# Kernel tuning notes

Measured on AMD Instinct MI355X. Metric: run time of the kernel, lower is better.

The kernel has to match this reference:

```python
import jax, jax.numpy as jnp
import numpy as np

N_COARSE = 12500
N_FINE = 50000
MIN_BASIS = 16  # (min(L_in, L_out) + 1) ** 2 with L_in = L_out = 3


def setup_inputs() -> dict:
    key = jax.random.key(0)
    ks = jax.random.split(key, 8)
    return {
        "last_inv": jax.random.normal(ks[0], (N_COARSE, 256), dtype=jnp.float32),
        "cur_inv": jax.random.normal(ks[1], (N_FINE, 256), dtype=jnp.float32),
        "last_equ": jax.random.normal(ks[2], (N_COARSE, 16, 256), dtype=jnp.float32),
        "cur_equ": jax.random.normal(ks[3], (N_FINE, 16, 256), dtype=jnp.float32),
        "upsampling": jax.random.randint(ks[4], (N_FINE,), 0, N_COARSE, dtype=jnp.int32),
        # Linear weights stored as [in, out] (torch weight is [out, in]; x @ W.T == x @ W_in_out)
        "W_last_equ": jax.random.normal(ks[5], (256, 256), dtype=jnp.float32) * 0.02,
        "W_cur_equ": jax.random.normal(ks[6], (256, 256), dtype=jnp.float32) * 0.02,
        "W_mlp": jax.random.normal(ks[7], (768, 512), dtype=jnp.float32) * 0.02,
    }


def reference(last_inv, cur_inv, last_equ, cur_equ, upsampling, W_last_equ, W_cur_equ, W_mlp):
    # nearest_upsample: gather coarse rows up to fine resolution
    li = jnp.take(last_inv, upsampling, axis=0)                 # [N_fine, 256]
    le = jnp.take(last_equ, upsampling, axis=0)[:, :MIN_BASIS]  # [N_fine, 16, 256]
    le = jnp.einsum('nbc,cd->nbd', le, W_last_equ)              # fc_last_equ (no bias)
    ce = jnp.einsum('nbc,cd->nbd', cur_equ[:, :MIN_BASIS], W_cur_equ)  # fc_cur_equ
    equ = (ce * le).mean(axis=1)                                # [N_fine, 256]
    com = jnp.concatenate([li, cur_inv, equ], axis=-1)          # [N_fine, 768]
    return com @ W_mlp                                          # LastUnaryBlock: Linear, no bias
```

## Files before the change

kernel.cpp:

```cpp
#include <hip/hip_runtime.h>
#include <hip/hip_bf16.h>

#define N_COARSE 12500
#define N_FINE   50000

typedef __bf16 bf16x8 __attribute__((ext_vector_type(8)));
typedef __bf16 bf16x4 __attribute__((ext_vector_type(4)));
typedef float  f32x4  __attribute__((ext_vector_type(4)));


__device__ __forceinline__ bf16x8 cvt8(f32x4 x, f32x4 y) {
    bf16x8 r;
    r[0] = (__bf16)x[0]; r[1] = (__bf16)x[1]; r[2] = (__bf16)x[2]; r[3] = (__bf16)x[3];
    r[4] = (__bf16)y[0]; r[5] = (__bf16)y[1]; r[6] = (__bf16)y[2]; r[7] = (__bf16)y[3];
    return r;
}

__device__ __forceinline__ int swz(int row, int byte) { return byte ^ ((row & 7) << 4); }

__device__ __forceinline__ void st_a(__bf16* lds, int row, int cs, bf16x8 v) {
    *(bf16x8*)((char*)lds + swz(row, row * 512 + cs * 16)) = v;
}
__device__ __forceinline__ bf16x8 ld_a(const __bf16* lds, int row, int ka) {
    return *(const bf16x8*)((const char*)lds + swz(row, row * 512 + ka * 2));
}

template<int NT>
__device__ __forceinline__ void stage_f32(const float* __restrict__ A, long row0,
                                          __bf16* lds, int tid, long maxrow) {
    const int r0 = tid >> 5, cs = tid & 31;
    constexpr int RPI = NT / 32;
    #pragma unroll
    for (int i = 0; i < 64 / RPI; ++i) {
        int row = r0 + i * RPI;
        long gr = row0 + row; if (gr > maxrow) gr = maxrow;
        const float* p = A + gr * 256 + cs * 8;
        f32x4 x = *(const f32x4*)p, y = *(const f32x4*)(p + 4);
        st_a(lds, row, cs, cvt8(x, y));
    }
}

__device__ __forceinline__ void mfma_tile(const __bf16* lds, const bf16x8* __restrict__ packB,
                                          int N, int c0, int ksb,
                                          f32x4 (&acc)[4][4], int lane) {
    const int g = lane >> 4, r15 = lane & 15;
    #pragma unroll
    for (int ks = 0; ks < 8; ++ks) {
        bf16x8 a[4];
        #pragma unroll
        for (int rt = 0; rt < 4; ++rt)
            a[rt] = ld_a(lds, rt * 16 + r15, ks * 32 + g * 8);
        const size_t kb = (size_t)((ksb + ks) * 4 + g) * N;
        #pragma unroll
        for (int ct = 0; ct < 4; ++ct) {
            bf16x8 b = packB[kb + c0 + ct * 16 + r15];
            #pragma unroll
            for (int rt = 0; rt < 4; ++rt)
                acc[rt][ct] = __builtin_amdgcn_mfma_f32_16x16x32_bf16(a[rt], b, acc[rt][ct], 0, 0, 0);
        }
    }
}

__global__ __launch_bounds__(256) void k_pack(const float* __restrict__ W,
                                              __bf16* __restrict__ dst, int K, int N) {
    int idx = blockIdx.x * 256 + threadIdx.x;
    if (idx >= K * N) return;
    int k = idx / N, n = idx % N;
    dst[((size_t)(k >> 3) * N + n) * 8 + (k & 7)] = (__bf16)W[(size_t)k * N + n];
}

__global__ __launch_bounds__(256) void k_cvt(const float* __restrict__ src,
                                             __bf16* __restrict__ dst, int n4) {
    int i = blockIdx.x * 256 + threadIdx.x;
    if (i >= n4) return;
    f32x4 v = ((const f32x4*)src)[i];
    bf16x4 o;
    o[0] = (__bf16)v[0]; o[1] = (__bf16)v[1]; o[2] = (__bf16)v[2]; o[3] = (__bf16)v[3];
    ((bf16x4*)dst)[i] = o;
}

__global__ __launch_bounds__(256) void k_coarse_equ(
    const float* __restrict__ last_equ, const bf16x8* __restrict__ packW,
    __bf16* __restrict__ LEp)
{
    __shared__ __attribute__((aligned(16))) __bf16 As[64 * 256];
    const int tid = threadIdx.x, lane = tid & 63, wid = tid >> 6;
    const long row0 = (long)blockIdx.x * 64;
    stage_f32<256>(last_equ, row0, As, tid, (long)N_COARSE * 16 - 1);
    __syncthreads();
    f32x4 acc[4][4] = {};
    mfma_tile(As, packW, 256, wid * 64, 0, acc, lane);
    #pragma unroll
    for (int rt = 0; rt < 4; ++rt) {
        int coarse = (int)(row0 >> 4) + rt;
        #pragma unroll
        for (int ct = 0; ct < 4; ++ct) {
            int cg = wid * 4 + ct;
            bf16x4 v;
            v[0] = (__bf16)acc[rt][ct][0]; v[1] = (__bf16)acc[rt][ct][1];
            v[2] = (__bf16)acc[rt][ct][2]; v[3] = (__bf16)acc[rt][ct][3];
            *(bf16x4*)(LEp + ((size_t)(coarse * 16 + cg) * 64 + lane) * 4) = v;
        }
    }
}

__global__ __launch_bounds__(256) void k_fine_equ(
    const float* __restrict__ cur_equ, const bf16x8* __restrict__ packW,
    const __bf16* __restrict__ LEp, const int* __restrict__ up,
    __bf16* __restrict__ equ)
{
    __shared__ __attribute__((aligned(16))) __bf16 As[64 * 256];
    const int tid = threadIdx.x, lane = tid & 63, wid = tid >> 6;
    const int n0 = blockIdx.x * 4;
    const long row0 = (long)blockIdx.x * 64;

    int cu[4];
    #pragma unroll
    for (int rt = 0; rt < 4; ++rt) cu[rt] = up[n0 + rt];

    stage_f32<256>(cur_equ, row0, As, tid, (long)N_FINE * 16 - 1);

    bf16x4 le[4][4];
    #pragma unroll
    for (int rt = 0; rt < 4; ++rt)
        #pragma unroll
        for (int ct = 0; ct < 4; ++ct)
            le[rt][ct] = *(const bf16x4*)(LEp +
                ((size_t)(cu[rt] * 16 + wid * 4 + ct) * 64 + lane) * 4);

    __syncthreads();
    f32x4 acc[4][4] = {};
    mfma_tile(As, packW, 256, wid * 64, 0, acc, lane);

    #pragma unroll
    for (int rt = 0; rt < 4; ++rt) {
        int n = n0 + rt;
        #pragma unroll
        for (int ct = 0; ct < 4; ++ct) {
            float s = acc[rt][ct][0] * (float)le[rt][ct][0]
                    + acc[rt][ct][1] * (float)le[rt][ct][1]
                    + acc[rt][ct][2] * (float)le[rt][ct][2]
                    + acc[rt][ct][3] * (float)le[rt][ct][3];
            s += __shfl_xor(s, 16, 64);
            s += __shfl_xor(s, 32, 64);
            if (lane < 16)
                equ[(size_t)n * 256 + wid * 64 + ct * 16 + lane] = (__bf16)(s * 0.0625f);
        }
    }
}

__global__ __launch_bounds__(512) void k_out(
    const __bf16* __restrict__ li_bf, const float* __restrict__ cur_inv,
    const __bf16* __restrict__ equ, const bf16x8* __restrict__ packW,
    const int* __restrict__ up, float* __restrict__ out)
{
    __shared__ __attribute__((aligned(16))) __bf16 As[64 * 256];
    const int tid = threadIdx.x, lane = tid & 63, wid = tid >> 6;
    const int row0 = blockIdx.x * 64;
    const int c0 = wid * 64;
    const int r0 = tid >> 5, cs = tid & 31;
    f32x4 acc[4][4] = {};

    #pragma unroll
    for (int i = 0; i < 4; ++i) {
        int row = r0 + i * 16;
        int gr = row0 + row; if (gr > N_FINE - 1) gr = N_FINE - 1;
        st_a(As, row, cs, *(const bf16x8*)(li_bf + (size_t)up[gr] * 256 + cs * 8));
    }
    __syncthreads();
    mfma_tile(As, packW, 512, c0, 0, acc, lane);
    __syncthreads();

    stage_f32<512>(cur_inv, row0, As, tid, N_FINE - 1);
    __syncthreads();
    mfma_tile(As, packW, 512, c0, 8, acc, lane);
    __syncthreads();

    #pragma unroll
    for (int i = 0; i < 4; ++i) {
        int row = r0 + i * 16;
        int gr = row0 + row; if (gr > N_FINE - 1) gr = N_FINE - 1;
        st_a(As, row, cs, *(const bf16x8*)(equ + (size_t)gr * 256 + cs * 8));
    }
    __syncthreads();
    mfma_tile(As, packW, 512, c0, 16, acc, lane);

    const int g = lane >> 4, r15 = lane & 15;
    #pragma unroll
    for (int rt = 0; rt < 4; ++rt)
        #pragma unroll
        for (int j = 0; j < 4; ++j) {
            int r = row0 + rt * 16 + g * 4 + j;
            if (r < N_FINE)
                #pragma unroll
                for (int ct = 0; ct < 4; ++ct)
                    out[(size_t)r * 512 + c0 + ct * 16 + r15] = acc[rt][ct][j];
        }
}

extern "C" void kernel_launch(void* const* d_in, const int* in_sizes, int n_in,
                              void* d_out, int out_size, void* d_ws, size_t ws_size,
                              hipStream_t stream) {
    const float* last_inv = (const float*)d_in[0];
    const float* cur_inv  = (const float*)d_in[1];
    const float* last_equ = (const float*)d_in[2];
    const float* cur_equ  = (const float*)d_in[3];
    const int*   up       = (const int*)d_in[4];
    const float* W_le     = (const float*)d_in[5];
    const float* W_ce     = (const float*)d_in[6];
    const float* W_mlp    = (const float*)d_in[7];
    float* out = (float*)d_out;

    char* w = (char*)d_ws;
    __bf16* LEp    = (__bf16*)w;  w += (size_t)N_COARSE * 16 * 256 * 2;
    __bf16* equ    = (__bf16*)w;  w += (size_t)N_FINE * 256 * 2;
    __bf16* li_bf  = (__bf16*)w;  w += (size_t)N_COARSE * 256 * 2;
    __bf16* packLE = (__bf16*)w;  w += (size_t)256 * 256 * 2;
    __bf16* packCE = (__bf16*)w;  w += (size_t)256 * 256 * 2;
    __bf16* packM  = (__bf16*)w;  w += (size_t)768 * 512 * 2;

    k_pack<<<256, 256, 0, stream>>>(W_le, packLE, 256, 256);
    k_pack<<<256, 256, 0, stream>>>(W_ce, packCE, 256, 256);
    k_pack<<<1536, 256, 0, stream>>>(W_mlp, packM, 768, 512);
    k_cvt<<<3125, 256, 0, stream>>>(last_inv, li_bf, N_COARSE * 256 / 4);

    k_coarse_equ<<<N_COARSE * 16 / 64, 256, 0, stream>>>(
        last_equ, (const bf16x8*)packLE, LEp);

    k_fine_equ<<<N_FINE / 4, 256, 0, stream>>>(
        cur_equ, (const bf16x8*)packCE, LEp, up, equ);

    k_out<<<(N_FINE + 63) / 64, 512, 0, stream>>>(
        li_bf, cur_inv, equ, (const bf16x8*)packM, up, out);
}
```

Measured before the change: 581.1 us.

## Make equ kernels persistent with double-buffered LDS prefetch; overlap staging in k_out

The coarse and fine equivariant kernels become persistent: each block walks a contiguous range of tiles. The next tile's fp32 rows are loaded into registers while the current tile runs its MFMAs, and the next tile goes into a second LDS buffer. k_out also double-buffers its three K-chunks so that global loads overlap the matrix math, and uses lighter barriers. This targets memory-latency stalls, at the cost of more registers and LDS per block, which may lower occupancy, and a fixed grid size.

```diff
diff --git a/kernel.cpp b/kernel.cpp
--- a/kernel.cpp
+++ b/kernel.cpp
@@ -16,6 +16,11 @@
     return r;
 }
 
+__device__ __forceinline__ void lds_barrier() {
+    asm volatile("s_waitcnt lgkmcnt(0)" ::: "memory");
+    __builtin_amdgcn_s_barrier();
+}
+
 __device__ __forceinline__ int swz(int row, int byte) { return byte ^ ((row & 7) << 4); }
 
 __device__ __forceinline__ void st_a(__bf16* lds, int row, int cs, bf16x8 v) {
@@ -26,18 +31,25 @@
 }
 
 template<int NT>
-__device__ __forceinline__ void stage_f32(const float* __restrict__ A, long row0,
-                                          __bf16* lds, int tid, long maxrow) {
+__device__ __forceinline__ void load_f32_tile(const float* __restrict__ A, long row0,
+                                              long maxrow, int tid, f32x4* x, f32x4* y) {
     const int r0 = tid >> 5, cs = tid & 31;
     constexpr int RPI = NT / 32;
     #pragma unroll
     for (int i = 0; i < 64 / RPI; ++i) {
-        int row = r0 + i * RPI;
-        long gr = row0 + row; if (gr > maxrow) gr = maxrow;
+        long gr = row0 + r0 + i * RPI; if (gr > maxrow) gr = maxrow;
         const float* p = A + gr * 256 + cs * 8;
-        f32x4 x = *(const f32x4*)p, y = *(const f32x4*)(p + 4);
-        st_a(lds, row, cs, cvt8(x, y));
-    }
+        x[i] = *(const f32x4*)p; y[i] = *(const f32x4*)(p + 4);
+    }
+}
+template<int NT>
+__device__ __forceinline__ void store_tile(__bf16* lds, int tid,
+                                           const f32x4* x, const f32x4* y) {
+    const int r0 = tid >> 5, cs = tid & 31;
+    constexpr int RPI = NT / 32;
+    #pragma unroll
+    for (int i = 0; i < 64 / RPI; ++i)
+        st_a(lds, r0 + i * RPI, cs, cvt8(x[i], y[i]));
 }
 
 __device__ __forceinline__ void mfma_tile(const __bf16* lds, const bf16x8* __restrict__ packB,
@@ -79,73 +91,100 @@
     ((bf16x4*)dst)[i] = o;
 }
 
-__global__ __launch_bounds__(256) void k_coarse_equ(
+__global__ __launch_bounds__(256, 2) void k_coarse_equ(
     const float* __restrict__ last_equ, const bf16x8* __restrict__ packW,
     __bf16* __restrict__ LEp)
 {
-    __shared__ __attribute__((aligned(16))) __bf16 As[64 * 256];
+    __shared__ __attribute__((aligned(16))) __bf16 As[2][64 * 256];
     const int tid = threadIdx.x, lane = tid & 63, wid = tid >> 6;
-    const long row0 = (long)blockIdx.x * 64;
-    stage_f32<256>(last_equ, row0, As, tid, (long)N_COARSE * 16 - 1);
-    __syncthreads();
-    f32x4 acc[4][4] = {};
-    mfma_tile(As, packW, 256, wid * 64, 0, acc, lane);
-    #pragma unroll
-    for (int rt = 0; rt < 4; ++rt) {
-        int coarse = (int)(row0 >> 4) + rt;
-        #pragma unroll
-        for (int ct = 0; ct < 4; ++ct) {
-            int cg = wid * 4 + ct;
-            bf16x4 v;
-            v[0] = (__bf16)acc[rt][ct][0]; v[1] = (__bf16)acc[rt][ct][1];
-            v[2] = (__bf16)acc[rt][ct][2]; v[3] = (__bf16)acc[rt][ct][3];
-            *(bf16x4*)(LEp + ((size_t)(coarse * 16 + cg) * 64 + lane) * 4) = v;
-        }
-    }
-}
-
-__global__ __launch_bounds__(256) void k_fine_equ(
+    const int NTILES = N_COARSE * 16 / 64;
+    const int per = (NTILES + gridDim.x - 1) / gridDim.x;
+    const int tbeg = blockIdx.x * per;
+    const int tend = min(tbeg + per, NTILES);
+    if (tbeg >= tend) return;
+    const long maxrow = (long)N_COARSE * 16 - 1;
+
+    f32x4 x[8], y[8];
+    load_f32_tile<256>(last_equ, (long)tbeg * 64, maxrow, tid, x, y);
+    store_tile<256>(As[0], tid, x, y);
+    int cur = 0;
+    for (int t = tbeg; t < tend; ++t) {
+        lds_barrier();
+        const bool hn = (t + 1 < tend);
+        if (hn) load_f32_tile<256>(last_equ, (long)(t + 1) * 64, maxrow, tid, x, y);
+        __builtin_amdgcn_sched_barrier(0);
+        f32x4 acc[4][4] = {};
+        mfma_tile(As[cur], packW, 256, wid * 64, 0, acc, lane);
+        #pragma unroll
+        for (int rt = 0; rt < 4; ++rt) {
+            int coarse = t * 4 + rt;
+            #pragma unroll
+            for (int ct = 0; ct < 4; ++ct) {
+                int cg = wid * 4 + ct;
+                bf16x4 v;
+                v[0] = (__bf16)acc[rt][ct][0]; v[1] = (__bf16)acc[rt][ct][1];
+                v[2] = (__bf16)acc[rt][ct][2]; v[3] = (__bf16)acc[rt][ct][3];
+                *(bf16x4*)(LEp + ((size_t)(coarse * 16 + cg) * 64 + lane) * 4) = v;
+            }
+        }
+        if (hn) store_tile<256>(As[cur ^ 1], tid, x, y);
+        cur ^= 1;
+    }
+}
+
+__global__ __launch_bounds__(256, 2) void k_fine_equ(
     const float* __restrict__ cur_equ, const bf16x8* __restrict__ packW,
     const __bf16* __restrict__ LEp, const int* __restrict__ up,
     __bf16* __restrict__ equ)
 {
-    __shared__ __attribute__((aligned(16))) __bf16 As[64 * 256];
+    __shared__ __attribute__((aligned(16))) __bf16 As[2][64 * 256];
     const int tid = threadIdx.x, lane = tid & 63, wid = tid >> 6;
-    const int n0 = blockIdx.x * 4;
-    const long row0 = (long)blockIdx.x * 64;
-
-    int cu[4];
-    #pragma unroll
-    for (int rt = 0; rt < 4; ++rt) cu[rt] = up[n0 + rt];
-
-    stage_f32<256>(cur_equ, row0, As, tid, (long)N_FINE * 16 - 1);
-
-    bf16x4 le[4][4];
-    #pragma unroll
-    for (int rt = 0; rt < 4; ++rt)
-        #pragma unroll
-        for (int ct = 0; ct < 4; ++ct)
-            le[rt][ct] = *(const bf16x4*)(LEp +
-                ((size_t)(cu[rt] * 16 + wid * 4 + ct) * 64 + lane) * 4);
-
-    __syncthreads();
-    f32x4 acc[4][4] = {};
-    mfma_tile(As, packW, 256, wid * 64, 0, acc, lane);
-
-    #pragma unroll
-    for (int rt = 0; rt < 4; ++rt) {
-        int n = n0 + rt;
-        #pragma unroll
-        for (int ct = 0; ct < 4; ++ct) {
-            float s = acc[rt][ct][0] * (float)le[rt][ct][0]
-                    + acc[rt][ct][1] * (float)le[rt][ct][1]
-                    + acc[rt][ct][2] * (float)le[rt][ct][2]
-                    + acc[rt][ct][3] * (float)le[rt][ct][3];
-            s += __shfl_xor(s, 16, 64);
-            s += __shfl_xor(s, 32, 64);
-            if (lane < 16)
-                equ[(size_t)n * 256 + wid * 64 + ct * 16 + lane] = (__bf16)(s * 0.0625f);
-        }
+    const int NTILES = N_FINE / 4;
+    const int per = (NTILES + gridDim.x - 1) / gridDim.x;
+    const int tbeg = blockIdx.x * per;
+    const int tend = min(tbeg + per, NTILES);
+    if (tbeg >= tend) return;
+    const long maxrow = (long)N_FINE * 16 - 1;
+
+    f32x4 x[8], y[8];
+    load_f32_tile<256>(cur_equ, (long)tbeg * 64, maxrow, tid, x, y);
+    store_tile<256>(As[0], tid, x, y);
+    int cur = 0;
+    for (int t = tbeg; t < tend; ++t) {
+        lds_barrier();
+        const bool hn = (t + 1 < tend);
+        if (hn) load_f32_tile<256>(cur_equ, (long)(t + 1) * 64, maxrow, tid, x, y);
+        const int n0 = t * 4;
+        int cu[4];
+        #pragma unroll
+        for (int rt = 0; rt < 4; ++rt) cu[rt] = up[n0 + rt];
+        bf16x4 le[4][4];
+        #pragma unroll
+        for (int rt = 0; rt < 4; ++rt)
+            #pragma unroll
+            for (int ct = 0; ct < 4; ++ct)
+                le[rt][ct] = *(const bf16x4*)(LEp +
+                    ((size_t)(cu[rt] * 16 + wid * 4 + ct) * 64 + lane) * 4);
+        __builtin_amdgcn_sched_barrier(0);
+        f32x4 acc[4][4] = {};
+        mfma_tile(As[cur], packW, 256, wid * 64, 0, acc, lane);
+        #pragma unroll
+        for (int rt = 0; rt < 4; ++rt) {
+            #pragma unroll
+            for (int ct = 0; ct < 4; ++ct) {
+                float s = acc[rt][ct][0] * (float)le[rt][ct][0]
+                        + acc[rt][ct][1] * (float)le[rt][ct][1]
+                        + acc[rt][ct][2] * (float)le[rt][ct][2]
+                        + acc[rt][ct][3] * (float)le[rt][ct][3];
+                s += __shfl_xor(s, 16, 64);
+                s += __shfl_xor(s, 32, 64);
+                if (lane < 16)
+                    equ[(size_t)(n0 + rt) * 256 + wid * 64 + ct * 16 + lane] =
+                        (__bf16)(s * 0.0625f);
+            }
+        }
+        if (hn) store_tile<256>(As[cur ^ 1], tid, x, y);
+        cur ^= 1;
     }
 }
 
@@ -154,36 +193,42 @@
     const __bf16* __restrict__ equ, const bf16x8* __restrict__ packW,
     const int* __restrict__ up, float* __restrict__ out)
 {
-    __shared__ __attribute__((aligned(16))) __bf16 As[64 * 256];
+    __shared__ __attribute__((aligned(16))) __bf16 As[2][64 * 256];
     const int tid = threadIdx.x, lane = tid & 63, wid = tid >> 6;
     const int row0 = blockIdx.x * 64;
+    const int r0 = tid >> 5, cs = tid & 31;
     const int c0 = wid * 64;
-    const int r0 = tid >> 5, cs = tid & 31;
     f32x4 acc[4][4] = {};
 
+    bf16x8 bz[4];
     #pragma unroll
     for (int i = 0; i < 4; ++i) {
-        int row = r0 + i * 16;
-        int gr = row0 + row; if (gr > N_FINE - 1) gr = N_FINE - 1;
-        st_a(As, row, cs, *(const bf16x8*)(li_bf + (size_t)up[gr] * 256 + cs * 8));
-    }
-    __syncthreads();
-    mfma_tile(As, packW, 512, c0, 0, acc, lane);
-    __syncthreads();
-
-    stage_f32<512>(cur_inv, row0, As, tid, N_FINE - 1);
-    __syncthreads();
-    mfma_tile(As, packW, 512, c0, 8, acc, lane);
-    __syncthreads();
-
+        int gr = row0 + r0 + i * 16; if (gr > N_FINE - 1) gr = N_FINE - 1;
+        bz[i] = *(const bf16x8*)(li_bf + (size_t)up[gr] * 256 + cs * 8);
+    }
+    #pragma unroll
+    for (int i = 0; i < 4; ++i) st_a(As[0], r0 + i * 16, cs, bz[i]);
+
+    lds_barrier();
+    f32x4 x[4], y[4];
+    load_f32_tile<512>(cur_inv, row0, N_FINE - 1, tid, x, y);
+    __builtin_amdgcn_sched_barrier(0);
+    mfma_tile(As[0], packW, 512, c0, 0, acc, lane);
+    store_tile<512>(As[1], tid, x, y);
+
+    lds_barrier();
     #pragma unroll
     for (int i = 0; i < 4; ++i) {
-        int row = r0 + i * 16;
-        int gr = row0 + row; if (gr > N_FINE - 1) gr = N_FINE - 1;
-        st_a(As, row, cs, *(const bf16x8*)(equ + (size_t)gr * 256 + cs * 8));
-    }
-    __syncthreads();
-    mfma_tile(As, packW, 512, c0, 16, acc, lane);
+        int gr = row0 + r0 + i * 16; if (gr > N_FINE - 1) gr = N_FINE - 1;
+        bz[i] = *(const bf16x8*)(equ + (size_t)gr * 256 + cs * 8);
+    }
+    __builtin_amdgcn_sched_barrier(0);
+    mfma_tile(As[1], packW, 512, c0, 8, acc, lane);
+    #pragma unroll
+    for (int i = 0; i < 4; ++i) st_a(As[0], r0 + i * 16, cs, bz[i]);
+
+    lds_barrier();
+    mfma_tile(As[0], packW, 512, c0, 16, acc, lane);
 
     const int g = lane >> 4, r15 = lane & 15;
     #pragma unroll
@@ -224,11 +269,9 @@
     k_pack<<<1536, 256, 0, stream>>>(W_mlp, packM, 768, 512);
     k_cvt<<<3125, 256, 0, stream>>>(last_inv, li_bf, N_COARSE * 256 / 4);
 
-    k_coarse_equ<<<N_COARSE * 16 / 64, 256, 0, stream>>>(
-        last_equ, (const bf16x8*)packLE, LEp);
-
-    k_fine_equ<<<N_FINE / 4, 256, 0, stream>>>(
-        cur_equ, (const bf16x8*)packCE, LEp, up, equ);
+    k_coarse_equ<<<625, 256, 0, stream>>>(last_equ, (const bf16x8*)packLE, LEp);
+
+    k_fine_equ<<<500, 256, 0, stream>>>(cur_equ, (const bf16x8*)packCE, LEp, up, equ);
 
     k_out<<<(N_FINE + 63) / 64, 512, 0, stream>>>(
         li_bf, cur_inv, equ, (const bf16x8*)packM, up, out);
```

Result: slower. 662.3 us (+14.0%).
